# Kernel tuning notes

Hardware: AMD Instinct MI355X
Metric: run time of the kernel (lower is better)

Reference implementation:

```python
import jax, jax.numpy as jnp
import numpy as np

B, T, D = 512, 200, 512

def setup_inputs() -> dict:
    key = jax.random.key(0)
    k1, k2, k3 = jax.random.split(key, 3)
    inputs = jax.random.normal(k1, (B, T, D), dtype=jnp.float32)
    # Keras 'uniform' initializer -> U(-0.05, 0.05)
    W = jax.random.uniform(k2, (T, T), minval=-0.05, maxval=0.05, dtype=jnp.float32)
    b = jax.random.uniform(k3, (T,), minval=-0.05, maxval=0.05, dtype=jnp.float32)
    return {"inputs": inputs, "W": W, "b": b}

def reference(inputs, W, b):
    # x = permute(inputs, (0,2,1)) -> [B, D, T]; scores over timestep axis
    # a = softmax(tanh(x @ W + b)) along last axis (T)
    scores = jnp.tanh(jnp.einsum('btd,ts->bds', inputs, W) + b)  # [B, D, T]
    a = jax.nn.softmax(scores, axis=-1)                           # softmax over T
    # permute back to [B, T, D], elementwise multiply, sum over T -> [B, D]
    out = jnp.einsum('bdt,btd->bd', a, inputs)
    return out
```

## Files before the change

### kernel.cpp

```cpp
#include <hip/hip_runtime.h>
#include <cstdint>
#include <cstddef>

#define B_DIM 512
#define T_DIM 200
#define D_DIM 512
#define NPAD  208
#define NKG   28
#define NT    13
#define KS_STEPS 7
#define SLICE 3208

typedef short  short8  __attribute__((ext_vector_type(8)));
typedef float  floatx4 __attribute__((ext_vector_type(4)));

__device__ __forceinline__ float bf2f(unsigned short h) {
  return __uint_as_float(((unsigned int)h) << 16);
}
__device__ __forceinline__ unsigned short f2bf(float f) {
  unsigned int u = __float_as_uint(f);
  u += 0x7fffu + ((u >> 16) & 1u);
  return (unsigned short)(u >> 16);
}
__device__ __forceinline__ unsigned int cvt_pk_bf16(float a, float b) {
  unsigned int d;
  asm("v_cvt_pk_bf16_f32 %0, %1, %2" : "=v"(d) : "v"(a), "v"(b));
  return d;
}

__global__ void prep_w_kernel(const float* __restrict__ W,
                              unsigned short* __restrict__ wf) {
  int idx = blockIdx.x * blockDim.x + threadIdx.x;
  if (idx >= NKG * 8 * NPAD) return;
  int k = idx / NPAD;
  int n = idx - k * NPAD;
  float v = (k < T_DIM && n < T_DIM) ? W[k * T_DIM + n] : 0.0f;
  wf[((size_t)(k >> 3) * NPAD + n) * 8 + (k & 7)] = f2bf(v);
}

__global__ __launch_bounds__(512, 4)
void attn_kernel(const float* __restrict__ X,
                 const unsigned short* __restrict__ wf,
                 const float* __restrict__ bias,
                 float* __restrict__ out) {
  __shared__ __align__(16) unsigned short Xa[2][4 * SLICE];
  __shared__ __align__(16) float comb[8][2][64][2];

  const int tid  = threadIdx.x;
  const int wv   = tid >> 6;
  const int lane = tid & 63;
  const int l15  = lane & 15;
  const int g    = lane >> 4;

  const int bb = blockIdx.x;

  const int c4 = tid & 15;
  const int t0 = tid >> 4;
  const float* src0 = X + (size_t)bb * (T_DIM * D_DIM)
                      + (size_t)t0 * D_DIM + (c4 << 2);
  const int dbase = (c4 >> 2) * SLICE
                  + ((t0 >> 3) * 16 + ((c4 & 3) << 2)) * 8 + (t0 & 7);

  const int nt0 = (wv < 5) ? 2 * wv : (wv + 5);
  const int ntw = (wv < 5) ? 2 : 1;

  float bb2[2];
  int   xb16[2];
  bool  val[2];
  #pragma unroll
  for (int j = 0; j < 2; ++j) {
    const int t = (nt0 + j) * 16 + l15;
    val[j] = (j < ntw) && (t < T_DIM);
    const int tc = (t < T_DIM) ? t : (T_DIM - 1);
    bb2[j]  = 2.0f * bias[tc];
    xb16[j] = ((tc >> 3) * 16) * 8 + (tc & 7);
  }

  const unsigned short* wk = wf + ((size_t)g * NPAD + nt0 * 16 + l15) * 8;

  float4 pf[7];
  #pragma unroll
  for (int it = 0; it < 7; ++it)
    if (it < 6 || tid < 128) pf[it] = *(const float4*)(src0 + (size_t)it * 32 * D_DIM);
  {
    unsigned short* dst = &Xa[0][dbase];
    #pragma unroll
    for (int it = 0; it < 7; ++it) {
      if (it < 6 || tid < 128) {
        unsigned int w01 = cvt_pk_bf16(pf[it].x, pf[it].y);
        unsigned int w23 = cvt_pk_bf16(pf[it].z, pf[it].w);
        dst[0]  = (unsigned short)(w01 & 0xffffu);
        dst[8]  = (unsigned short)(w01 >> 16);
        dst[16] = (unsigned short)(w23 & 0xffffu);
        dst[24] = (unsigned short)(w23 >> 16);
      }
      dst += 512;
    }
  }
  __syncthreads();

  #pragma unroll 2
  for (int n = 0; n < 8; ++n) {
    const int cur = n & 1;
    const unsigned short* Xw = &Xa[cur][0];

    floatx4 acc[4][2];
    #pragma unroll
    for (int h = 0; h < 4; ++h)
      #pragma unroll
      for (int j = 0; j < 2; ++j)
        acc[h][j] = (floatx4){0.f, 0.f, 0.f, 0.f};

    #pragma unroll
    for (int ks = 0; ks < KS_STEPS; ++ks) {
      const int kg = ks * 4 + g;
      short8 b0 = *(const short8*)(wk + (size_t)ks * (4 * NPAD * 8));
      short8 b1;
      if (ntw == 2) b1 = *(const short8*)(wk + (size_t)ks * (4 * NPAD * 8) + 128);
      const bool av = (ks < 6) || (g == 0);
      short8 a[4];
      #pragma unroll
      for (int h = 0; h < 4; ++h)
        a[h] = av ? *(const short8*)&Xw[h * SLICE + (kg * 16 + l15) * 8]
                  : (short8){0, 0, 0, 0, 0, 0, 0, 0};
      #pragma unroll
      for (int h = 0; h < 4; ++h)
        acc[h][0] = __builtin_amdgcn_mfma_f32_16x16x32_bf16(a[h], b0, acc[h][0], 0, 0, 0);
      if (ntw == 2) {
        #pragma unroll
        for (int h = 0; h < 4; ++h)
          acc[h][1] = __builtin_amdgcn_mfma_f32_16x16x32_bf16(a[h], b1, acc[h][1], 0, 0, 0);
      }
    }

    if (n < 7) {
      const float* src = src0 + ((n + 1) << 6);
      #pragma unroll
      for (int it = 0; it < 7; ++it)
        if (it < 6 || tid < 128) pf[it] = *(const float4*)(src + (size_t)it * 32 * D_DIM);
    }

    float part[4][4], rs[4][4];
    #pragma unroll
    for (int h = 0; h < 4; ++h)
      #pragma unroll
      for (int r = 0; r < 4; ++r) { part[h][r] = 0.f; rs[h][r] = 0.f; }

    #pragma unroll
    for (int j = 0; j < 2; ++j) {
      if (j < ntw) {
        const unsigned short* xp = &Xw[xb16[j]];
        #pragma unroll
        for (int r = 0; r < 4; ++r) {
          const int m = g * 4 + r;
          #pragma unroll
          for (int h = 0; h < 4; ++h) {
            float u  = __expf(__builtin_fmaf(acc[h][j][r], 2.0f, bb2[j]));
            float v  = __fdividef(2.0f, u + 1.0f);
            float p  = val[j] ? __expf(-v) : 0.0f;
            rs[h][r]   += p;
            part[h][r] += p * bf2f(xp[h * SLICE + m * 8]);
          }
        }
      }
    }
    #pragma unroll
    for (int off = 1; off <= 4; off <<= 1)
      #pragma unroll
      for (int h = 0; h < 4; ++h)
        #pragma unroll
        for (int r = 0; r < 4; ++r) {
          part[h][r] += __shfl_xor(part[h][r], off, 16);
          rs[h][r]   += __shfl_xor(rs[h][r],   off, 16);
        }
    if ((l15 & 7) == 0) {
      const int q = l15 >> 3;
      #pragma unroll
      for (int h = 0; h < 4; ++h)
        #pragma unroll
        for (int r = 0; r < 4; ++r) {
          const int idx = h * 16 + g * 4 + r;
          comb[wv][q][idx][0] = part[h][r];
          comb[wv][q][idx][1] = rs[h][r];
        }
    }
    __syncthreads();

    if (tid < 64) {
      float ps = 0.f, ss = 0.f;
      #pragma unroll
      for (int w = 0; w < 8; ++w)
        #pragma unroll
        for (int q = 0; q < 2; ++q) {
          const float2 v = *(const float2*)&comb[w][q][tid][0];
          ps += v.x;
          ss += v.y;
        }
      out[(size_t)bb * D_DIM + (n << 6) + tid] = ps * __frcp_rn(ss);
    }

    if (n < 7) {
      unsigned short* dst = &Xa[cur ^ 1][dbase];
      #pragma unroll
      for (int it = 0; it < 7; ++it) {
        if (it < 6 || tid < 128) {
          unsigned int w01 = cvt_pk_bf16(pf[it].x, pf[it].y);
          unsigned int w23 = cvt_pk_bf16(pf[it].z, pf[it].w);
          dst[0]  = (unsigned short)(w01 & 0xffffu);
          dst[8]  = (unsigned short)(w01 >> 16);
          dst[16] = (unsigned short)(w23 & 0xffffu);
          dst[24] = (unsigned short)(w23 >> 16);
        }
        dst += 512;
      }
      __syncthreads();
    }
  }
}

extern "C" void kernel_launch(void* const* d_in, const int* in_sizes, int n_in,
                              void* d_out, int out_size, void* d_ws, size_t ws_size,
                              hipStream_t stream) {
  const float* X  = (const float*)d_in[0];
  const float* W  = (const float*)d_in[1];
  const float* bs = (const float*)d_in[2];
  float* out = (float*)d_out;
  unsigned short* wf = (unsigned short*)d_ws;

  const int wtot = NKG * 8 * NPAD;
  hipLaunchKernelGGL(prep_w_kernel, dim3((wtot + 255) / 256), dim3(256), 0, stream,
                     W, wf);
  hipLaunchKernelGGL(attn_kernel, dim3(512), dim3(512), 0, stream,
                     X, wf, bs, out);
}
```

Measured before the change: 350.6 us.

## Single-buffer X tile, keep W fragments in registers, raise MFMA priority

Replaces the double-buffered LDS X staging and its register prefetch with a single LDS buffer that is loaded synchronously at the top of each D-chunk iteration. The W fragments for all k-steps are hoisted into registers once instead of being reloaded from global memory every iteration. s_setprio raises wave priority around the MFMA loop, and the softmax/accumulate epilogue is restructured per h to shrink live registers. This halves LDS use and cuts register pressure to allow more resident blocks, but it gives up the overlap of global loads with compute inside a block and relies on other blocks to hide latency.

```diff
diff --git a/kernel.cpp b/kernel.cpp
--- a/kernel.cpp
+++ b/kernel.cpp
@@ -43,7 +43,7 @@
                  const unsigned short* __restrict__ wf,
                  const float* __restrict__ bias,
                  float* __restrict__ out) {
-  __shared__ __align__(16) unsigned short Xa[2][4 * SLICE];
+  __shared__ __align__(16) unsigned short Xs[4 * SLICE];
   __shared__ __align__(16) float comb[8][2][64][2];
 
   const int tid  = threadIdx.x;
@@ -53,13 +53,6 @@
   const int g    = lane >> 4;
 
   const int bb = blockIdx.x;
-
-  const int c4 = tid & 15;
-  const int t0 = tid >> 4;
-  const float* src0 = X + (size_t)bb * (T_DIM * D_DIM)
-                      + (size_t)t0 * D_DIM + (c4 << 2);
-  const int dbase = (c4 >> 2) * SLICE
-                  + ((t0 >> 3) * 16 + ((c4 & 3) << 2)) * 8 + (t0 & 7);
 
   const int nt0 = (wv < 5) ? 2 * wv : (wv + 5);
   const int ntw = (wv < 5) ? 2 : 1;
@@ -70,137 +63,38 @@
   #pragma unroll
   for (int j = 0; j < 2; ++j) {
     const int t = (nt0 + j) * 16 + l15;
-    val[j] = (j < ntw) && (t < T_DIM);
+    val[j] = (t < T_DIM);
     const int tc = (t < T_DIM) ? t : (T_DIM - 1);
     bb2[j]  = 2.0f * bias[tc];
     xb16[j] = ((tc >> 3) * 16) * 8 + (tc & 7);
   }
 
   const unsigned short* wk = wf + ((size_t)g * NPAD + nt0 * 16 + l15) * 8;
-
-  float4 pf[7];
+  short8 bA[7], bB[7];
   #pragma unroll
-  for (int it = 0; it < 7; ++it)
-    if (it < 6 || tid < 128) pf[it] = *(const float4*)(src0 + (size_t)it * 32 * D_DIM);
-  {
-    unsigned short* dst = &Xa[0][dbase];
-    #pragma unroll
-    for (int it = 0; it < 7; ++it) {
-      if (it < 6 || tid < 128) {
-        unsigned int w01 = cvt_pk_bf16(pf[it].x, pf[it].y);
-        unsigned int w23 = cvt_pk_bf16(pf[it].z, pf[it].w);
-        dst[0]  = (unsigned short)(w01 & 0xffffu);
-        dst[8]  = (unsigned short)(w01 >> 16);
-        dst[16] = (unsigned short)(w23 & 0xffffu);
-        dst[24] = (unsigned short)(w23 >> 16);
-      }
-      dst += 512;
-    }
+  for (int ks = 0; ks < KS_STEPS; ++ks) {
+    bA[ks] = *(const short8*)(wk + (size_t)ks * (4 * NPAD * 8));
+    if (ntw == 2)
+      bB[ks] = *(const short8*)(wk + (size_t)ks * (4 * NPAD * 8) + 128);
   }
-  __syncthreads();
-
-  #pragma unroll 2
+
+  const int c4 = tid & 15;
+  const int t0 = tid >> 4;
+  const float* srcb = X + (size_t)bb * (T_DIM * D_DIM)
+                      + (size_t)t0 * D_DIM + (c4 << 2);
+  const int dbase = (c4 >> 2) * SLICE
+                  + ((t0 >> 3) * 16 + ((c4 & 3) << 2)) * 8 + (t0 & 7);
+
+  #pragma unroll 1
   for (int n = 0; n < 8; ++n) {
-    const int cur = n & 1;
-    const unsigned short* Xw = &Xa[cur][0];
-
-    floatx4 acc[4][2];
-    #pragma unroll
-    for (int h = 0; h < 4; ++h)
-      #pragma unroll
-      for (int j = 0; j < 2; ++j)
-        acc[h][j] = (floatx4){0.f, 0.f, 0.f, 0.f};
-
-    #pragma unroll
-    for (int ks = 0; ks < KS_STEPS; ++ks) {
-      const int kg = ks * 4 + g;
-      short8 b0 = *(const short8*)(wk + (size_t)ks * (4 * NPAD * 8));
-      short8 b1;
-      if (ntw == 2) b1 = *(const short8*)(wk + (size_t)ks * (4 * NPAD * 8) + 128);
-      const bool av = (ks < 6) || (g == 0);
-      short8 a[4];
-      #pragma unroll
-      for (int h = 0; h < 4; ++h)
-        a[h] = av ? *(const short8*)&Xw[h * SLICE + (kg * 16 + l15) * 8]
-                  : (short8){0, 0, 0, 0, 0, 0, 0, 0};
-      #pragma unroll
-      for (int h = 0; h < 4; ++h)
-        acc[h][0] = __builtin_amdgcn_mfma_f32_16x16x32_bf16(a[h], b0, acc[h][0], 0, 0, 0);
-      if (ntw == 2) {
-        #pragma unroll
-        for (int h = 0; h < 4; ++h)
-          acc[h][1] = __builtin_amdgcn_mfma_f32_16x16x32_bf16(a[h], b1, acc[h][1], 0, 0, 0);
-      }
-    }
-
-    if (n < 7) {
-      const float* src = src0 + ((n + 1) << 6);
+    {
+      const float* src = srcb + (n << 6);
+      float4 pf[7];
       #pragma unroll
       for (int it = 0; it < 7; ++it)
-        if (it < 6 || tid < 128) pf[it] = *(const float4*)(src + (size_t)it * 32 * D_DIM);
-    }
-
-    float part[4][4], rs[4][4];
-    #pragma unroll
-    for (int h = 0; h < 4; ++h)
-      #pragma unroll
-      for (int r = 0; r < 4; ++r) { part[h][r] = 0.f; rs[h][r] = 0.f; }
-
-    #pragma unroll
-    for (int j = 0; j < 2; ++j) {
-      if (j < ntw) {
-        const unsigned short* xp = &Xw[xb16[j]];
-        #pragma unroll
-        for (int r = 0; r < 4; ++r) {
-          const int m = g * 4 + r;
-          #pragma unroll
-          for (int h = 0; h < 4; ++h) {
-            float u  = __expf(__builtin_fmaf(acc[h][j][r], 2.0f, bb2[j]));
-            float v  = __fdividef(2.0f, u + 1.0f);
-            float p  = val[j] ? __expf(-v) : 0.0f;
-            rs[h][r]   += p;
-            part[h][r] += p * bf2f(xp[h * SLICE + m * 8]);
-          }
-        }
-      }
-    }
-    #pragma unroll
-    for (int off = 1; off <= 4; off <<= 1)
-      #pragma unroll
-      for (int h = 0; h < 4; ++h)
-        #pragma unroll
-        for (int r = 0; r < 4; ++r) {
-          part[h][r] += __shfl_xor(part[h][r], off, 16);
-          rs[h][r]   += __shfl_xor(rs[h][r],   off, 16);
-        }
-    if ((l15 & 7) == 0) {
-      const int q = l15 >> 3;
-      #pragma unroll
-      for (int h = 0; h < 4; ++h)
-        #pragma unroll
-        for (int r = 0; r < 4; ++r) {
-          const int idx = h * 16 + g * 4 + r;
-          comb[wv][q][idx][0] = part[h][r];
-          comb[wv][q][idx][1] = rs[h][r];
-        }
-    }
-    __syncthreads();
-
-    if (tid < 64) {
-      float ps = 0.f, ss = 0.f;
-      #pragma unroll
-      for (int w = 0; w < 8; ++w)
-        #pragma unroll
-        for (int q = 0; q < 2; ++q) {
-          const float2 v = *(const float2*)&comb[w][q][tid][0];
-          ps += v.x;
-          ss += v.y;
-        }
-      out[(size_t)bb * D_DIM + (n << 6) + tid] = ps * __frcp_rn(ss);
-    }
-
-    if (n < 7) {
-      unsigned short* dst = &Xa[cur ^ 1][dbase];
+        if (it < 6 || tid < 128)
+          pf[it] = *(const float4*)(src + (size_t)it * 32 * D_DIM);
+      unsigned short* dst = &Xs[dbase];
       #pragma unroll
       for (int it = 0; it < 7; ++it) {
         if (it < 6 || tid < 128) {
@@ -213,7 +107,85 @@
         }
         dst += 512;
       }
-      __syncthreads();
+    }
+    __syncthreads();
+
+    floatx4 acc[4][2];
+    #pragma unroll
+    for (int h = 0; h < 4; ++h)
+      #pragma unroll
+      for (int j = 0; j < 2; ++j)
+        acc[h][j] = (floatx4){0.f, 0.f, 0.f, 0.f};
+
+    __builtin_amdgcn_s_setprio(1);
+    #pragma unroll
+    for (int ks = 0; ks < KS_STEPS; ++ks) {
+      const int kg = ks * 4 + g;
+      const bool av = (ks < 6) || (g == 0);
+      short8 a[4];
+      #pragma unroll
+      for (int h = 0; h < 4; ++h)
+        a[h] = av ? *(const short8*)&Xs[h * SLICE + (kg * 16 + l15) * 8]
+                  : (short8){0, 0, 0, 0, 0, 0, 0, 0};
+      #pragma unroll
+      for (int h = 0; h < 4; ++h)
+        acc[h][0] = __builtin_amdgcn_mfma_f32_16x16x32_bf16(a[h], bA[ks], acc[h][0], 0, 0, 0);
+      if (ntw == 2) {
+        #pragma unroll
+        for (int h = 0; h < 4; ++h)
+          acc[h][1] = __builtin_amdgcn_mfma_f32_16x16x32_bf16(a[h], bB[ks], acc[h][1], 0, 0, 0);
+      }
+    }
+    __builtin_amdgcn_s_setprio(0);
+
+    #pragma unroll
+    for (int h = 0; h < 4; ++h) {
+      float part[4] = {0.f, 0.f, 0.f, 0.f};
+      float rs[4]   = {0.f, 0.f, 0.f, 0.f};
+      #pragma unroll
+      for (int j = 0; j < 2; ++j) {
+        if (j < ntw) {
+          const unsigned short* xp = &Xs[h * SLICE + xb16[j]];
+          #pragma unroll
+          for (int r = 0; r < 4; ++r) {
+            float u = __expf(__builtin_fmaf(acc[h][j][r], 2.0f, bb2[j]));
+            float v = __fdividef(2.0f, u + 1.0f);
+            float p = val[j] ? __expf(-v) : 0.0f;
+            rs[r]   += p;
+            part[r] += p * bf2f(xp[(g * 4 + r) * 8]);
+          }
+        }
+      }
+      #pragma unroll
+      for (int off = 1; off <= 4; off <<= 1)
+        #pragma unroll
+        for (int r = 0; r < 4; ++r) {
+          part[r] += __shfl_xor(part[r], off, 16);
+          rs[r]   += __shfl_xor(rs[r],   off, 16);
+        }
+      if ((l15 & 7) == 0) {
+        const int q = l15 >> 3;
+        #pragma unroll
+        for (int r = 0; r < 4; ++r) {
+          const int idx = h * 16 + g * 4 + r;
+          comb[wv][q][idx][0] = part[r];
+          comb[wv][q][idx][1] = rs[r];
+        }
+      }
+    }
+    __syncthreads();
+
+    if (tid < 64) {
+      float ps = 0.f, ss = 0.f;
+      #pragma unroll
+      for (int w = 0; w < 8; ++w)
+        #pragma unroll
+        for (int q = 0; q < 2; ++q) {
+          const float2 v = *(const float2*)&comb[w][q][tid][0];
+          ps += v.x;
+          ss += v.y;
+        }
+      out[(size_t)bb * D_DIM + (n << 6) + tid] = ps * __frcp_rn(ss);
     }
   }
 }
```

After: 308.9 us. -11.9%, faster.
